# Optimization experiments

Hardware: AMD Instinct MI355X
Metric: run time of the kernel (lower is better)

Reference implementation:

```python
import jax, jax.numpy as jnp
import numpy as np

N_NODES = 50000
N_EDGES = 800000
IN_DIM = 128
HIDDEN = 128
OUT_DIM = 64


def setup_inputs() -> dict:
    key = jax.random.key(0)
    ks = jax.random.split(key, 10)
    x = jax.random.normal(ks[0], (N_NODES, IN_DIM), dtype=jnp.float32)
    edge_index = jax.random.randint(ks[1], (2, N_EDGES), 0, N_NODES, dtype=jnp.int64)
    def lin(k, fan_in, fan_out):
        bound = 1.0 / np.sqrt(fan_in)
        kw, kb = jax.random.split(k)
        W = jax.random.uniform(kw, (fan_in, fan_out), jnp.float32, -bound, bound)
        b = jax.random.uniform(kb, (fan_out,), jnp.float32, -bound, bound)
        return W, b
    W1, b1 = lin(ks[2], IN_DIM, HIDDEN)   # gcn layer 1
    W2, b2 = lin(ks[3], HIDDEN, HIDDEN)   # gcn layer 2
    W3, b3 = lin(ks[4], HIDDEN, HIDDEN)   # post_mp linear 1
    W4, b4 = lin(ks[5], HIDDEN, OUT_DIM)  # post_mp linear 2
    return {"x": x, "edge_index": edge_index,
            "W1": W1, "b1": b1, "W2": W2, "b2": b2,
            "W3": W3, "b3": b3, "W4": W4, "b4": b4}


def reference(x, edge_index, W1, b1, W2, b2, W3, b3, W4, b4):
    N = x.shape[0]
    # add self-loops (matches convert_to_adj)
    loops = jnp.arange(N, dtype=edge_index.dtype)
    row = jnp.concatenate([edge_index[0], loops])  # destination / adj row
    col = jnp.concatenate([edge_index[1], loops])  # source / adj col
    # row-normalization: vals = 1 / deg(row), deg from scatter-add of ones
    deg = jax.ops.segment_sum(jnp.ones(row.shape[0], x.dtype), row, num_segments=N)
    vals = 1.0 / deg[row]  # [E+N]

    def propagate(h):
        # SpMM: out[i] = sum_j A_norm[i,j] * h[j]  via gather-scale-scatter
        return jax.ops.segment_sum(vals[:, None] * h[col], row, num_segments=N)

    # layer 1: spmm -> linear -> relu (dropout is identity in eval mode)
    h = jax.nn.relu(propagate(x) @ W1 + b1)
    # layer 2
    h = jax.nn.relu(propagate(h) @ W2 + b2)
    # post_mp: Linear -> Dropout(eval=identity) -> Linear
    h = h @ W3 + b3
    return h @ W4 + b4
```

## Files before the change

kernel.cpp:

```cpp
#include <hip/hip_runtime.h>
#include <hip/hip_bf16.h>

#define NB 512

typedef __attribute__((ext_vector_type(8))) short short8_t;
typedef __attribute__((ext_vector_type(8))) unsigned short ushort8_t;
typedef __attribute__((ext_vector_type(4))) float f32x4;

__device__ inline unsigned short bf16_rne(float f) {
    union { float f; unsigned u; } x; x.f = f;
    unsigned r = x.u + 0x7fffu + ((x.u >> 16) & 1u);
    return (unsigned short)(r >> 16);
}
__device__ inline float bf16_to_f32(unsigned short h) {
    union { unsigned u; float f; } x; x.u = ((unsigned)h) << 16;
    return x.f;
}
__device__ __forceinline__ void acc_uint2(float& a0, float& a1, float& a2, float& a3, uint2 v) {
    a0 += bf16_to_f32((unsigned short)(v.x & 0xffff));
    a1 += bf16_to_f32((unsigned short)(v.x >> 16));
    a2 += bf16_to_f32((unsigned short)(v.y & 0xffff));
    a3 += bf16_to_f32((unsigned short)(v.y >> 16));
}


template <int NC, bool OUT_BF16>
__device__ __forceinline__ void gemm_core(const unsigned short* __restrict__ As,
                                          const unsigned short* __restrict__ Wt,
                                          const float* __restrict__ gemm_bias,
                                          void* __restrict__ Cout, int row0, int n) {
    constexpr int CT = NC / 32;
    const int t = threadIdx.x;
    const int w = t >> 6;
    const int l = t & 63;
    const int col = l & 15;
    const int kg = l >> 4;
    const int arow = (w & 3) * 16 + col;
    const int cbase = (w >> 2) * (NC / 2);
    const int abase = arow * 256;
    const int axor = (arow & 7) << 4;

    short8_t afrag[4];
#pragma unroll
    for (int ks = 0; ks < 4; ++ks) {
        int abyte = abase + ((ks * 64 + kg * 16) ^ axor);
        afrag[ks] = *(const short8_t*)((const char*)As + abyte);
    }

    f32x4 acc[CT];
#pragma unroll
    for (int ct = 0; ct < CT; ++ct) acc[ct] = (f32x4){0.f, 0.f, 0.f, 0.f};

#pragma unroll
    for (int ct = 0; ct < CT; ++ct) {
        const unsigned short* wp = Wt + (size_t)(cbase + ct * 16 + col) * 128 + kg * 8;
#pragma unroll
        for (int ks = 0; ks < 4; ++ks) {
            short8_t b = *(const short8_t*)(wp + ks * 32);
            acc[ct] = __builtin_amdgcn_mfma_f32_16x16x32_bf16(afrag[ks], b, acc[ct], 0, 0, 0);
        }
    }

    const int orow0 = row0 + (w & 3) * 16 + kg * 4;
    if (OUT_BF16) {
        unsigned short* C = (unsigned short*)Cout;
#pragma unroll
        for (int ct = 0; ct < CT; ++ct) {
#pragma unroll
            for (int j = 0; j < 4; ++j) {
                C[(size_t)(orow0 + j) * NC + cbase + ct * 16 + col] = bf16_rne(acc[ct][j]);
            }
        }
    } else {
        float* C = (float*)Cout;
#pragma unroll
        for (int ct = 0; ct < CT; ++ct) {
            float b = (gemm_bias != nullptr) ? gemm_bias[cbase + ct * 16 + col] : 0.f;
#pragma unroll
            for (int j = 0; j < 4; ++j) {
                int r = orow0 + j;
                if (r < n) C[(size_t)r * NC + cbase + ct * 16 + col] = acc[ct][j] + b;
            }
        }
    }
}


__global__ __launch_bounds__(512) void prep_p0_k(const int* __restrict__ e_row, int E, int R,
                                                 int* __restrict__ bucket_cnt, int pb,
                                                 const float* __restrict__ W1,
                                                 const float* __restrict__ W2,
                                                 const float* __restrict__ W3,
                                                 const float* __restrict__ b3,
                                                 const float* __restrict__ W4,
                                                 const float* __restrict__ b4,
                                                 unsigned short* __restrict__ w1t,
                                                 unsigned short* __restrict__ w2t,
                                                 unsigned short* __restrict__ wft,
                                                 float* __restrict__ bfv) {
    __shared__ int h[NB];
    if ((int)blockIdx.x < pb) {
        for (int i = threadIdx.x; i < NB; i += 512) h[i] = 0;
        __syncthreads();
        int base = blockIdx.x * 8192;
#pragma unroll
        for (int j = 0; j < 16; ++j) {
            int i = base + j * 512 + threadIdx.x;
            if (i < E) atomicAdd(&h[e_row[i] / R], 1);
        }
        __syncthreads();
        for (int i = threadIdx.x; i < NB; i += 512)
            if (h[i]) atomicAdd(&bucket_cnt[i], h[i]);
    } else {
        int idx = (blockIdx.x - pb) * 512 + threadIdx.x;
        if (idx < 16384) {
            int k = idx >> 7, c = idx & 127;
            w1t[c * 128 + k] = bf16_rne(W1[idx]);
        } else if (idx < 32768) {
            int j = idx - 16384;
            int k = j >> 7, c = j & 127;
            w2t[c * 128 + k] = bf16_rne(W2[j]);
        } else if (idx < 40960) {
            int j = idx - 32768;
            int k = j >> 6, o = j & 63;
            float acc = 0.f;
            for (int m = 0; m < 128; ++m) acc = fmaf(W3[k * 128 + m], W4[m * 64 + o], acc);
            wft[o * 128 + k] = bf16_rne(acc);
        } else if (idx < 41024) {
            int o = idx - 40960;
            float acc = b4[o];
            for (int m = 0; m < 128; ++m) acc = fmaf(b3[m], W4[m * 64 + o], acc);
            bfv[o] = acc;
        }
    }
}


__global__ __launch_bounds__(512) void gemm1_p0b_k(const float* __restrict__ x,
                                                   const unsigned short* __restrict__ w1t,
                                                   unsigned short* __restrict__ t1, int n, int gb,
                                                   const int* __restrict__ bucket_cnt,
                                                   int* __restrict__ bptr, int* __restrict__ bcur,
                                                   int E) {
    __shared__ char smem[16384];
    if ((int)blockIdx.x < gb) {
        unsigned short* As = (unsigned short*)smem;
        const int t = threadIdx.x;
        const int row0 = blockIdx.x * 64;
#pragma unroll
        for (int it = 0; it < 2; ++it) {
            int idx = it * 4096 + t * 8;
            int rl = idx >> 7;
            int cl = idx & 127;
            int gr = row0 + rl; if (gr > n - 1) gr = n - 1;
            const float4* src = (const float4*)(x + (size_t)gr * 128 + cl);
            float4 v0 = src[0];
            float4 v1 = src[1];
            float f[8] = {v0.x, v0.y, v0.z, v0.w, v1.x, v1.y, v1.z, v1.w};
            ushort8_t vh;
#pragma unroll
            for (int j = 0; j < 8; ++j) vh[j] = bf16_rne(f[j]);
            int byte = rl * 256 + ((cl * 2) ^ ((rl & 7) << 4));
            *(ushort8_t*)(smem + byte) = vh;
        }
        __syncthreads();
        gemm_core<128, true>(As, w1t, nullptr, t1, row0, n);
    } else {
        int* s = (int*)smem;
        int t = threadIdx.x;
        int v = bucket_cnt[t];
        s[t] = v;
        __syncthreads();
        for (int off = 1; off < NB; off <<= 1) {
            int u = (t >= off) ? s[t - off] : 0;
            __syncthreads();
            s[t] += u;
            __syncthreads();
        }
        int excl = s[t] - v;
        bptr[t] = excl;
        bcur[t] = excl;
        if (t == NB - 1) bptr[NB] = E;
    }
}


__global__ __launch_bounds__(256) void p1_scatter_k(const int* __restrict__ er,
                                                    const int* __restrict__ ec, int E, int R,
                                                    int* __restrict__ bcur,
                                                    unsigned* __restrict__ packed) {
    __shared__ int h[NB];
    __shared__ int base[NB];
    for (int i = threadIdx.x; i < NB; i += 256) h[i] = 0;
    __syncthreads();
    int cb = blockIdx.x * 4096;
    int rows[16], cols[16], bks[16];
#pragma unroll
    for (int j = 0; j < 16; ++j) {
        int i = cb + j * 256 + threadIdx.x;
        if (i < E) {
            int r = er[i];
            rows[j] = r;
            cols[j] = ec[i];
            int b = r / R;
            bks[j] = b;
            atomicAdd(&h[b], 1);
        } else {
            bks[j] = -1;
        }
    }
    __syncthreads();
    for (int i = threadIdx.x; i < NB; i += 256)
        base[i] = h[i] ? atomicAdd(&bcur[i], h[i]) : 0;
    __syncthreads();
    for (int i = threadIdx.x; i < NB; i += 256) h[i] = 0;
    __syncthreads();
#pragma unroll
    for (int j = 0; j < 16; ++j) {
        int b = bks[j];
        if (b >= 0) {
            int off = atomicAdd(&h[b], 1);
            packed[base[b] + off] = ((unsigned)(rows[j] - b * R) << 16) | (unsigned)cols[j];
        }
    }
}


__global__ __launch_bounds__(256) void p2_build_k(const unsigned* __restrict__ packed,
                                                  const int* __restrict__ bptr, int R, int N, int E,
                                                  int* __restrict__ row_ptr,
                                                  float* __restrict__ deginv,
                                                  int* __restrict__ csr_col) {
    __shared__ int hist[128];
    __shared__ int excl[129];
    __shared__ int cur[128];
    __shared__ int lcsr[2048];
    int b = blockIdx.x;
    int s = bptr[b], e = bptr[b + 1];
    int m = e - s;
    for (int i = threadIdx.x; i < 128; i += 256) hist[i] = 0;
    __syncthreads();
    for (int i = threadIdx.x; i < m; i += 256) atomicAdd(&hist[packed[s + i] >> 16], 1);
    __syncthreads();
    if (threadIdx.x == 0) {
        int acc = 0;
        for (int r = 0; r < R; ++r) { excl[r] = acc; acc += hist[r]; }
        excl[R] = acc;
    }
    __syncthreads();
    for (int r = threadIdx.x; r < R; r += 256) {
        int gr = b * R + r;
        if (gr < N) {
            row_ptr[gr] = s + excl[r];
            deginv[gr] = 1.0f / (float)(hist[r] + 1);
        }
        cur[r] = excl[r];
    }
    if (b == (int)gridDim.x - 1 && threadIdx.x == 0) row_ptr[N] = E;
    __syncthreads();
    if (m <= 2048) {
        for (int i = threadIdx.x; i < m; i += 256) {
            unsigned pk = packed[s + i];
            int pos = atomicAdd(&cur[pk >> 16], 1);
            lcsr[pos] = (int)(pk & 0xffffu);
        }
        __syncthreads();
        for (int i = threadIdx.x; i < m; i += 256) csr_col[s + i] = lcsr[i];
    } else {
        for (int i = threadIdx.x; i < m; i += 256) {
            unsigned pk = packed[s + i];
            int pos = atomicAdd(&cur[pk >> 16], 1);
            csr_col[s + pos] = (int)(pk & 0xffffu);
        }
    }
}


template <int NC, bool OUT_BF16>
__global__ __launch_bounds__(512) void fused_agg_gemm_k(const unsigned short* __restrict__ tin,
                                                        const int* __restrict__ row_ptr,
                                                        const int* __restrict__ csr_col,
                                                        const float* __restrict__ deginv,
                                                        const float* __restrict__ agg_bias,
                                                        const unsigned short* __restrict__ Wt,
                                                        const float* __restrict__ gemm_bias,
                                                        void* __restrict__ Cout, int n) {
    __shared__ unsigned short As[64 * 128];
    __shared__ int cols_s[2048];
    __shared__ int rp_s[65];
    __shared__ float di_s[64];
    const int t = threadIdx.x;
    const int row0 = blockIdx.x * 64;
    const int w = t >> 6;
    const int l = t & 63;
    const int half = l >> 5;
    const int sl = l & 31;
    const uint2* tw = (const uint2*)tin;
    const float4 bb = ((const float4*)agg_bias)[sl];

    if (t < 65) {
        int gr = row0 + t; if (gr > n) gr = n;
        rp_s[t] = row_ptr[gr];
    } else if (t < 129) {
        int gr = row0 + (t - 65); if (gr > n - 1) gr = n - 1;
        di_s[t - 65] = deginv[gr];
    }
    __syncthreads();
    const int seg0 = rp_s[0];
    {
        int seg_len = rp_s[64] - seg0;
        if (seg_len > 2048) seg_len = 2048;
        for (int i = t; i < seg_len; i += 512) cols_s[i] = csr_col[seg0 + i];
    }
    __syncthreads();

#pragma unroll
    for (int it = 0; it < 4; ++it) {
        int rl = it * 16 + w * 2 + half;
        int grow = row0 + rl; if (grow > n - 1) grow = n - 1;
        uint2 sv = tw[(size_t)grow * 32 + sl];
        float a0 = bf16_to_f32((unsigned short)(sv.x & 0xffff));
        float a1 = bf16_to_f32((unsigned short)(sv.x >> 16));
        float a2 = bf16_to_f32((unsigned short)(sv.y & 0xffff));
        float a3 = bf16_to_f32((unsigned short)(sv.y >> 16));
        const int s = rp_s[rl], e = rp_s[rl + 1];
        const int d = e - s;
        if (e - seg0 <= 2048) {
            const int loc = s - seg0;
            int p = 0;
            for (; p + 8 <= d; p += 8) {
                int c0 = cols_s[loc + p + 0];
                int c1 = cols_s[loc + p + 1];
                int c2 = cols_s[loc + p + 2];
                int c3 = cols_s[loc + p + 3];
                int c4 = cols_s[loc + p + 4];
                int c5 = cols_s[loc + p + 5];
                int c6 = cols_s[loc + p + 6];
                int c7 = cols_s[loc + p + 7];
                uint2 v0 = tw[(size_t)c0 * 32 + sl];
                uint2 v1 = tw[(size_t)c1 * 32 + sl];
                uint2 v2 = tw[(size_t)c2 * 32 + sl];
                uint2 v3 = tw[(size_t)c3 * 32 + sl];
                uint2 v4 = tw[(size_t)c4 * 32 + sl];
                uint2 v5 = tw[(size_t)c5 * 32 + sl];
                uint2 v6 = tw[(size_t)c6 * 32 + sl];
                uint2 v7 = tw[(size_t)c7 * 32 + sl];
                acc_uint2(a0, a1, a2, a3, v0);
                acc_uint2(a0, a1, a2, a3, v1);
                acc_uint2(a0, a1, a2, a3, v2);
                acc_uint2(a0, a1, a2, a3, v3);
                acc_uint2(a0, a1, a2, a3, v4);
                acc_uint2(a0, a1, a2, a3, v5);
                acc_uint2(a0, a1, a2, a3, v6);
                acc_uint2(a0, a1, a2, a3, v7);
            }
            for (; p < d; ++p) {
                int c = cols_s[loc + p];
                uint2 v = tw[(size_t)c * 32 + sl];
                acc_uint2(a0, a1, a2, a3, v);
            }
        } else {
            for (int p = s; p < e; ++p) {
                int c = csr_col[p];
                uint2 v = tw[(size_t)c * 32 + sl];
                acc_uint2(a0, a1, a2, a3, v);
            }
        }
        float di = di_s[rl];
        float r0 = fmaxf(fmaf(a0, di, bb.x), 0.f);
        float r1 = fmaxf(fmaf(a1, di, bb.y), 0.f);
        float r2 = fmaxf(fmaf(a2, di, bb.z), 0.f);
        float r3 = fmaxf(fmaf(a3, di, bb.w), 0.f);
        uint2 pk;
        pk.x = (unsigned)bf16_rne(r0) | ((unsigned)bf16_rne(r1) << 16);
        pk.y = (unsigned)bf16_rne(r2) | ((unsigned)bf16_rne(r3) << 16);
        int byte = rl * 256 + ((sl * 8) ^ ((rl & 7) << 4));
        *(uint2*)((char*)As + byte) = pk;
    }
    __syncthreads();

    gemm_core<NC, OUT_BF16>(As, Wt, gemm_bias, Cout, row0, n);
}


extern "C" void kernel_launch(void* const* d_in, const int* in_sizes, int n_in,
                              void* d_out, int out_size, void* d_ws, size_t ws_size,
                              hipStream_t stream) {
    const float* x  = (const float*)d_in[0];
    const int* edges = (const int*)d_in[1];
    const float* W1 = (const float*)d_in[2];
    const float* b1 = (const float*)d_in[3];
    const float* W2 = (const float*)d_in[4];
    const float* b2 = (const float*)d_in[5];
    const float* W3 = (const float*)d_in[6];
    const float* b3 = (const float*)d_in[7];
    const float* W4 = (const float*)d_in[8];
    const float* b4 = (const float*)d_in[9];

    const int N = in_sizes[0] / 128;
    const int E = in_sizes[1] / 2;
    const int NPAD = (N + 63) & ~63;
    const int R = (N + NB - 1) / NB;
    const int* e_row = edges;
    const int* e_col = edges + E;

    char* p = (char*)d_ws;
    auto alloc = [&](size_t bytes) {
        void* r = (void*)p;
        p += (bytes + 255) & ~(size_t)255;
        return r;
    };
    unsigned short* t_bf = (unsigned short*)alloc((size_t)NPAD * 128 * 2);
    unsigned short* t2_bf = (unsigned short*)alloc((size_t)NPAD * 128 * 2);
    float* deginv  = (float*)alloc((size_t)N * 4);
    int*   row_ptr = (int*)alloc((size_t)(N + 1) * 4);
    int*   csr_col = (int*)alloc((size_t)E * 4);
    unsigned* packed = (unsigned*)alloc((size_t)E * 4);
    int*   bucket_cnt = (int*)alloc(NB * 4);
    int*   bucket_ptr = (int*)alloc((NB + 1) * 4);
    int*   bucket_cur = (int*)alloc(NB * 4);
    unsigned short* w1t = (unsigned short*)alloc(128 * 128 * 2);
    unsigned short* w2t = (unsigned short*)alloc(128 * 128 * 2);
    unsigned short* wft = (unsigned short*)alloc(64 * 128 * 2);
    float* bfv     = (float*)alloc(64 * 4);

    float* out = (float*)d_out;

    hipMemsetAsync(bucket_cnt, 0, NB * 4, stream);

    const int PB = (E + 8191) / 8192;
    const int WB = (41024 + 511) / 512;
    const int gblocks = NPAD / 64;

    prep_p0_k<<<PB + WB, 512, 0, stream>>>(e_row, E, R, bucket_cnt, PB,
                                           W1, W2, W3, b3, W4, b4, w1t, w2t, wft, bfv);
    gemm1_p0b_k<<<gblocks + 1, 512, 0, stream>>>(x, w1t, t_bf, N, gblocks,
                                                 bucket_cnt, bucket_ptr, bucket_cur, E);
    p1_scatter_k<<<(E + 4095) / 4096, 256, 0, stream>>>(e_row, e_col, E, R, bucket_cur, packed);
    p2_build_k<<<NB, 256, 0, stream>>>(packed, bucket_ptr, R, N, E, row_ptr, deginv, csr_col);

    fused_agg_gemm_k<128, true><<<gblocks, 512, 0, stream>>>(
        t_bf, row_ptr, csr_col, deginv, b1, w2t, nullptr, t2_bf, N);
    fused_agg_gemm_k<64, false><<<gblocks, 512, 0, stream>>>(
        t2_bf, row_ptr, csr_col, deginv, b2, wft, bfv, out, N);
}
```

Measured before the change: 221.3 us.

## Partition CSR by source-column chunk to improve gather locality

Edges are bucketed by source-column chunk (4 chunks of 12800 nodes) as well as by destination row block. This produces four per-chunk row pointer arrays, so aggregation walks neighbours chunk by chunk and its gathers concentrate on a smaller slice of the feature table at a time, aiming for better L2 reuse. Degree inverse is now computed inline from the summed chunk degrees instead of being stored, and the gather loop uses two accumulator sets. It adds more buckets, a larger scan, extra row-pointer loads, and a hardcoded chunk size that assumes N at most 51200.

Result: slower. 270.7 us (+22.3%).

```diff
diff --git a/kernel.cpp b/kernel.cpp
--- a/kernel.cpp
+++ b/kernel.cpp
@@ -2,6 +2,9 @@
 #include <hip/hip_bf16.h>
 
 #define NB 512
+#define NCHUNK 4
+#define NBK (NB * NCHUNK)
+#define CHUNK_ROWS 12800
 
 typedef __attribute__((ext_vector_type(8))) short short8_t;
 typedef __attribute__((ext_vector_type(8))) unsigned short ushort8_t;
@@ -86,7 +89,8 @@
 }
 
 
-__global__ __launch_bounds__(512) void prep_p0_k(const int* __restrict__ e_row, int E, int R,
+__global__ __launch_bounds__(512) void prep_p0_k(const int* __restrict__ e_row,
+                                                 const int* __restrict__ e_col, int E, int R,
                                                  int* __restrict__ bucket_cnt, int pb,
                                                  const float* __restrict__ W1,
                                                  const float* __restrict__ W2,
@@ -98,18 +102,21 @@
                                                  unsigned short* __restrict__ w2t,
                                                  unsigned short* __restrict__ wft,
                                                  float* __restrict__ bfv) {
-    __shared__ int h[NB];
+    __shared__ int h[NBK];
     if ((int)blockIdx.x < pb) {
-        for (int i = threadIdx.x; i < NB; i += 512) h[i] = 0;
+        for (int i = threadIdx.x; i < NBK; i += 512) h[i] = 0;
         __syncthreads();
         int base = blockIdx.x * 8192;
 #pragma unroll
         for (int j = 0; j < 16; ++j) {
             int i = base + j * 512 + threadIdx.x;
-            if (i < E) atomicAdd(&h[e_row[i] / R], 1);
+            if (i < E) {
+                int bk = (e_col[i] / CHUNK_ROWS) * NB + e_row[i] / R;
+                atomicAdd(&h[bk], 1);
+            }
         }
         __syncthreads();
-        for (int i = threadIdx.x; i < NB; i += 512)
+        for (int i = threadIdx.x; i < NBK; i += 512)
             if (h[i]) atomicAdd(&bucket_cnt[i], h[i]);
     } else {
         int idx = (blockIdx.x - pb) * 512 + threadIdx.x;
@@ -168,41 +175,49 @@
     } else {
         int* s = (int*)smem;
         int t = threadIdx.x;
-        int v = bucket_cnt[t];
-        s[t] = v;
+        int t4 = t * 4;
+        int v0 = bucket_cnt[t4 + 0];
+        int v1 = bucket_cnt[t4 + 1];
+        int v2 = bucket_cnt[t4 + 2];
+        int v3 = bucket_cnt[t4 + 3];
+        int tsum = v0 + v1 + v2 + v3;
+        s[t] = tsum;
         __syncthreads();
-        for (int off = 1; off < NB; off <<= 1) {
+        for (int off = 1; off < 512; off <<= 1) {
             int u = (t >= off) ? s[t - off] : 0;
             __syncthreads();
             s[t] += u;
             __syncthreads();
         }
-        int excl = s[t] - v;
-        bptr[t] = excl;
-        bcur[t] = excl;
-        if (t == NB - 1) bptr[NB] = E;
-    }
-}
-
-
-__global__ __launch_bounds__(256) void p1_scatter_k(const int* __restrict__ er,
+        int excl = s[t] - tsum;
+        bptr[t4 + 0] = excl;            bcur[t4 + 0] = excl;
+        bptr[t4 + 1] = excl + v0;       bcur[t4 + 1] = excl + v0;
+        bptr[t4 + 2] = excl + v0 + v1;  bcur[t4 + 2] = excl + v0 + v1;
+        bptr[t4 + 3] = excl + v0 + v1 + v2; bcur[t4 + 3] = excl + v0 + v1 + v2;
+        if (t == 511) bptr[NBK] = E;
+    }
+}
+
+
+__global__ __launch_bounds__(512) void p1_scatter_k(const int* __restrict__ er,
                                                     const int* __restrict__ ec, int E, int R,
                                                     int* __restrict__ bcur,
                                                     unsigned* __restrict__ packed) {
-    __shared__ int h[NB];
-    __shared__ int base[NB];
-    for (int i = threadIdx.x; i < NB; i += 256) h[i] = 0;
-    __syncthreads();
-    int cb = blockIdx.x * 4096;
+    __shared__ int h[NBK];
+    __shared__ int base[NBK];
+    for (int i = threadIdx.x; i < NBK; i += 512) h[i] = 0;
+    __syncthreads();
+    int cb = blockIdx.x * 8192;
     int rows[16], cols[16], bks[16];
 #pragma unroll
     for (int j = 0; j < 16; ++j) {
-        int i = cb + j * 256 + threadIdx.x;
+        int i = cb + j * 512 + threadIdx.x;
         if (i < E) {
             int r = er[i];
+            int c = ec[i];
             rows[j] = r;
-            cols[j] = ec[i];
-            int b = r / R;
+            cols[j] = c;
+            int b = (c / CHUNK_ROWS) * NB + r / R;
             bks[j] = b;
             atomicAdd(&h[b], 1);
         } else {
@@ -210,17 +225,18 @@
         }
     }
     __syncthreads();
-    for (int i = threadIdx.x; i < NB; i += 256)
+    for (int i = threadIdx.x; i < NBK; i += 512)
         base[i] = h[i] ? atomicAdd(&bcur[i], h[i]) : 0;
     __syncthreads();
-    for (int i = threadIdx.x; i < NB; i += 256) h[i] = 0;
+    for (int i = threadIdx.x; i < NBK; i += 512) h[i] = 0;
     __syncthreads();
 #pragma unroll
     for (int j = 0; j < 16; ++j) {
         int b = bks[j];
         if (b >= 0) {
             int off = atomicAdd(&h[b], 1);
-            packed[base[b] + off] = ((unsigned)(rows[j] - b * R) << 16) | (unsigned)cols[j];
+            int localrow = rows[j] - (b & (NB - 1)) * R;
+            packed[base[b] + off] = ((unsigned)localrow << 16) | (unsigned)cols[j];
         }
     }
 }
@@ -228,14 +244,15 @@
 
 __global__ __launch_bounds__(256) void p2_build_k(const unsigned* __restrict__ packed,
                                                   const int* __restrict__ bptr, int R, int N, int E,
-                                                  int* __restrict__ row_ptr,
-                                                  float* __restrict__ deginv,
+                                                  int* __restrict__ rp2,
                                                   int* __restrict__ csr_col) {
     __shared__ int hist[128];
     __shared__ int excl[129];
     __shared__ int cur[128];
     __shared__ int lcsr[2048];
     int b = blockIdx.x;
+    int c = b / NB;
+    int rb = b & (NB - 1);
     int s = bptr[b], e = bptr[b + 1];
     int m = e - s;
     for (int i = threadIdx.x; i < 128; i += 256) hist[i] = 0;
@@ -249,14 +266,11 @@
     }
     __syncthreads();
     for (int r = threadIdx.x; r < R; r += 256) {
-        int gr = b * R + r;
-        if (gr < N) {
-            row_ptr[gr] = s + excl[r];
-            deginv[gr] = 1.0f / (float)(hist[r] + 1);
-        }
+        int gr = rb * R + r;
+        if (gr < N) rp2[(size_t)c * N + gr] = s + excl[r];
         cur[r] = excl[r];
     }
-    if (b == (int)gridDim.x - 1 && threadIdx.x == 0) row_ptr[N] = E;
+    if (b == NBK - 1 && threadIdx.x == 0) rp2[(size_t)NCHUNK * N] = E;
     __syncthreads();
     if (m <= 2048) {
         for (int i = threadIdx.x; i < m; i += 256) {
@@ -278,17 +292,15 @@
 
 template <int NC, bool OUT_BF16>
 __global__ __launch_bounds__(512) void fused_agg_gemm_k(const unsigned short* __restrict__ tin,
-                                                        const int* __restrict__ row_ptr,
+                                                        const int* __restrict__ rp2,
                                                         const int* __restrict__ csr_col,
-                                                        const float* __restrict__ deginv,
                                                         const float* __restrict__ agg_bias,
                                                         const unsigned short* __restrict__ Wt,
                                                         const float* __restrict__ gemm_bias,
                                                         void* __restrict__ Cout, int n) {
     __shared__ unsigned short As[64 * 128];
     __shared__ int cols_s[2048];
-    __shared__ int rp_s[65];
-    __shared__ float di_s[64];
+    __shared__ int rp_s[NCHUNK][65];
     const int t = threadIdx.x;
     const int row0 = blockIdx.x * 64;
     const int w = t >> 6;
@@ -298,19 +310,26 @@
     const uint2* tw = (const uint2*)tin;
     const float4 bb = ((const float4*)agg_bias)[sl];
 
-    if (t < 65) {
-        int gr = row0 + t; if (gr > n) gr = n;
-        rp_s[t] = row_ptr[gr];
-    } else if (t < 129) {
-        int gr = row0 + (t - 65); if (gr > n - 1) gr = n - 1;
-        di_s[t - 65] = deginv[gr];
-    }
-    __syncthreads();
-    const int seg0 = rp_s[0];
-    {
-        int seg_len = rp_s[64] - seg0;
-        if (seg_len > 2048) seg_len = 2048;
-        for (int i = t; i < seg_len; i += 512) cols_s[i] = csr_col[seg0 + i];
+    if (t < NCHUNK * 65) {
+        int c = t / 65, i = t - c * 65;
+        int mi = row0 + i; if (mi > n) mi = n;
+        rp_s[c][i] = rp2[(size_t)c * n + mi];
+    }
+    __syncthreads();
+
+    int off_c[NCHUNK + 1];
+    off_c[0] = 0;
+#pragma unroll
+    for (int c = 0; c < NCHUNK; ++c) off_c[c + 1] = off_c[c] + (rp_s[c][64] - rp_s[c][0]);
+    const bool staged = off_c[NCHUNK] <= 2048;
+    if (staged) {
+#pragma unroll
+        for (int c = 0; c < NCHUNK; ++c) {
+            int s0 = rp_s[c][0];
+            int len = rp_s[c][64] - s0;
+            int o = off_c[c];
+            for (int i = t; i < len; i += 512) cols_s[o + i] = csr_col[s0 + i];
+        }
     }
     __syncthreads();
 
@@ -323,50 +342,45 @@
         float a1 = bf16_to_f32((unsigned short)(sv.x >> 16));
         float a2 = bf16_to_f32((unsigned short)(sv.y & 0xffff));
         float a3 = bf16_to_f32((unsigned short)(sv.y >> 16));
-        const int s = rp_s[rl], e = rp_s[rl + 1];
-        const int d = e - s;
-        if (e - seg0 <= 2048) {
-            const int loc = s - seg0;
-            int p = 0;
-            for (; p + 8 <= d; p += 8) {
-                int c0 = cols_s[loc + p + 0];
-                int c1 = cols_s[loc + p + 1];
-                int c2 = cols_s[loc + p + 2];
-                int c3 = cols_s[loc + p + 3];
-                int c4 = cols_s[loc + p + 4];
-                int c5 = cols_s[loc + p + 5];
-                int c6 = cols_s[loc + p + 6];
-                int c7 = cols_s[loc + p + 7];
-                uint2 v0 = tw[(size_t)c0 * 32 + sl];
-                uint2 v1 = tw[(size_t)c1 * 32 + sl];
-                uint2 v2 = tw[(size_t)c2 * 32 + sl];
-                uint2 v3 = tw[(size_t)c3 * 32 + sl];
-                uint2 v4 = tw[(size_t)c4 * 32 + sl];
-                uint2 v5 = tw[(size_t)c5 * 32 + sl];
-                uint2 v6 = tw[(size_t)c6 * 32 + sl];
-                uint2 v7 = tw[(size_t)c7 * 32 + sl];
-                acc_uint2(a0, a1, a2, a3, v0);
-                acc_uint2(a0, a1, a2, a3, v1);
-                acc_uint2(a0, a1, a2, a3, v2);
-                acc_uint2(a0, a1, a2, a3, v3);
-                acc_uint2(a0, a1, a2, a3, v4);
-                acc_uint2(a0, a1, a2, a3, v5);
-                acc_uint2(a0, a1, a2, a3, v6);
-                acc_uint2(a0, a1, a2, a3, v7);
+        float b0 = 0.f, b1 = 0.f, b2 = 0.f, b3v = 0.f;
+        int dtot = 0;
+#pragma unroll
+        for (int c = 0; c < NCHUNK; ++c) {
+            const int s = rp_s[c][rl], e = rp_s[c][rl + 1];
+            const int d = e - s;
+            dtot += d;
+            if (staged) {
+                const int base = off_c[c] + (s - rp_s[c][0]);
+                int p = 0;
+                for (; p + 4 <= d; p += 4) {
+                    int c0 = cols_s[base + p + 0];
+                    int c1 = cols_s[base + p + 1];
+                    int c2 = cols_s[base + p + 2];
+                    int c3 = cols_s[base + p + 3];
+                    uint2 v0 = tw[(size_t)c0 * 32 + sl];
+                    uint2 v1 = tw[(size_t)c1 * 32 + sl];
+                    uint2 v2 = tw[(size_t)c2 * 32 + sl];
+                    uint2 v3 = tw[(size_t)c3 * 32 + sl];
+                    acc_uint2(a0, a1, a2, a3, v0);
+                    acc_uint2(b0, b1, b2, b3v, v1);
+                    acc_uint2(a0, a1, a2, a3, v2);
+                    acc_uint2(b0, b1, b2, b3v, v3);
+                }
+                for (; p < d; ++p) {
+                    int cc = cols_s[base + p];
+                    uint2 v = tw[(size_t)cc * 32 + sl];
+                    acc_uint2(a0, a1, a2, a3, v);
+                }
+            } else {
+                for (int p = s; p < e; ++p) {
+                    int cc = csr_col[p];
+                    uint2 v = tw[(size_t)cc * 32 + sl];
+                    acc_uint2(a0, a1, a2, a3, v);
+                }
             }
-            for (; p < d; ++p) {
-                int c = cols_s[loc + p];
-                uint2 v = tw[(size_t)c * 32 + sl];
-                acc_uint2(a0, a1, a2, a3, v);
-            }
-        } else {
-            for (int p = s; p < e; ++p) {
-                int c = csr_col[p];
-                uint2 v = tw[(size_t)c * 32 + sl];
-                acc_uint2(a0, a1, a2, a3, v);
-            }
-        }
-        float di = di_s[rl];
+        }
+        a0 += b0; a1 += b1; a2 += b2; a3 += b3v;
+        float di = 1.0f / (float)(dtot + 1);
         float r0 = fmaxf(fmaf(a0, di, bb.x), 0.f);
         float r1 = fmaxf(fmaf(a1, di, bb.y), 0.f);
         float r2 = fmaxf(fmaf(a2, di, bb.z), 0.f);
@@ -412,13 +426,12 @@
     };
     unsigned short* t_bf = (unsigned short*)alloc((size_t)NPAD * 128 * 2);
     unsigned short* t2_bf = (unsigned short*)alloc((size_t)NPAD * 128 * 2);
-    float* deginv  = (float*)alloc((size_t)N * 4);
-    int*   row_ptr = (int*)alloc((size_t)(N + 1) * 4);
+    int*   rp2     = (int*)alloc(((size_t)NCHUNK * N + 1) * 4);
     int*   csr_col = (int*)alloc((size_t)E * 4);
     unsigned* packed = (unsigned*)alloc((size_t)E * 4);
-    int*   bucket_cnt = (int*)alloc(NB * 4);
-    int*   bucket_ptr = (int*)alloc((NB + 1) * 4);
-    int*   bucket_cur = (int*)alloc(NB * 4);
+    int*   bucket_cnt = (int*)alloc(NBK * 4);
+    int*   bucket_ptr = (int*)alloc((NBK + 1) * 4);
+    int*   bucket_cur = (int*)alloc(NBK * 4);
     unsigned short* w1t = (unsigned short*)alloc(128 * 128 * 2);
     unsigned short* w2t = (unsigned short*)alloc(128 * 128 * 2);
     unsigned short* wft = (unsigned short*)alloc(64 * 128 * 2);
@@ -426,21 +439,21 @@
 
     float* out = (float*)d_out;
 
-    hipMemsetAsync(bucket_cnt, 0, NB * 4, stream);
+    hipMemsetAsync(bucket_cnt, 0, NBK * 4, stream);
 
     const int PB = (E + 8191) / 8192;
     const int WB = (41024 + 511) / 512;
     const int gblocks = NPAD / 64;
 
-    prep_p0_k<<<PB + WB, 512, 0, stream>>>(e_row, E, R, bucket_cnt, PB,
+    prep_p0_k<<<PB + WB, 512, 0, stream>>>(e_row, e_col, E, R, bucket_cnt, PB,
                                            W1, W2, W3, b3, W4, b4, w1t, w2t, wft, bfv);
     gemm1_p0b_k<<<gblocks + 1, 512, 0, stream>>>(x, w1t, t_bf, N, gblocks,
                                                  bucket_cnt, bucket_ptr, bucket_cur, E);
-    p1_scatter_k<<<(E + 4095) / 4096, 256, 0, stream>>>(e_row, e_col, E, R, bucket_cur, packed);
-    p2_build_k<<<NB, 256, 0, stream>>>(packed, bucket_ptr, R, N, E, row_ptr, deginv, csr_col);
+    p1_scatter_k<<<(E + 8191) / 8192, 512, 0, stream>>>(e_row, e_col, E, R, bucket_cur, packed);
+    p2_build_k<<<NBK, 256, 0, stream>>>(packed, bucket_ptr, R, N, E, rp2, csr_col);
 
     fused_agg_gemm_k<128, true><<<gblocks, 512, 0, stream>>>(
-        t_bf, row_ptr, csr_col, deginv, b1, w2t, nullptr, t2_bf, N);
+        t_bf, rp2, csr_col, b1, w2t, nullptr, t2_bf, N);
     fused_agg_gemm_k<64, false><<<gblocks, 512, 0, stream>>>(
-        t2_bf, row_ptr, csr_col, deginv, b2, wft, bfv, out, N);
-}
+        t2_bf, rp2, csr_col, b2, wft, bfv, out, N);
+}
```

## Split fused aggregate-GEMM into slab-layout aggregation and separate GEMM kernels

Applied to the files above, without the earlier changes.

Stores the bf16 node features in four 32-column slabs (feature-group major) so each aggregation block gathers only 64-byte rows of one slab, which may improve cache locality of the random neighbour gathers. The fused aggregate+GEMM kernel is replaced by a separate aggregation kernel (four blocks per 64-row tile, one per slab) and a GEMM kernel that loads the slab tile into LDS with global_load_lds. This adds two extra launches and a round trip of the hidden activations through global memory, and it gathers the column indices four times.

Measured after the change: 231.3 us. 1.05x slower.

```diff
diff --git a/kernel.cpp b/kernel.cpp
--- a/kernel.cpp
+++ b/kernel.cpp
@@ -24,11 +24,11 @@
 }
 
 
-template <int NC, bool OUT_BF16>
+template <int NC, bool OUT_SLAB, bool SLAB_A>
 __device__ __forceinline__ void gemm_core(const unsigned short* __restrict__ As,
                                           const unsigned short* __restrict__ Wt,
                                           const float* __restrict__ gemm_bias,
-                                          void* __restrict__ Cout, int row0, int n) {
+                                          void* __restrict__ Cout, int row0, int n, int npad) {
     constexpr int CT = NC / 32;
     const int t = threadIdx.x;
     const int w = t >> 6;
@@ -37,13 +37,13 @@
     const int kg = l >> 4;
     const int arow = (w & 3) * 16 + col;
     const int cbase = (w >> 2) * (NC / 2);
-    const int abase = arow * 256;
-    const int axor = (arow & 7) << 4;
 
     short8_t afrag[4];
 #pragma unroll
     for (int ks = 0; ks < 4; ++ks) {
-        int abyte = abase + ((ks * 64 + kg * 16) ^ axor);
+        int abyte;
+        if (SLAB_A) abyte = ks * 4096 + arow * 64 + kg * 16;
+        else        abyte = arow * 256 + ((ks * 64 + kg * 16) ^ ((arow & 7) << 4));
         afrag[ks] = *(const short8_t*)((const char*)As + abyte);
     }
 
@@ -62,13 +62,15 @@
     }
 
     const int orow0 = row0 + (w & 3) * 16 + kg * 4;
-    if (OUT_BF16) {
+    if (OUT_SLAB) {
         unsigned short* C = (unsigned short*)Cout;
 #pragma unroll
         for (int ct = 0; ct < CT; ++ct) {
+            int f = cbase + ct * 16 + col;
+            unsigned short* slab = C + (size_t)(f >> 5) * npad * 32 + (f & 31);
 #pragma unroll
             for (int j = 0; j < 4; ++j) {
-                C[(size_t)(orow0 + j) * NC + cbase + ct * 16 + col] = bf16_rne(acc[ct][j]);
+                slab[(size_t)(orow0 + j) * 32] = bf16_rne(acc[ct][j]);
             }
         }
     } else {
@@ -138,8 +140,8 @@
 
 __global__ __launch_bounds__(512) void gemm1_p0b_k(const float* __restrict__ x,
                                                    const unsigned short* __restrict__ w1t,
-                                                   unsigned short* __restrict__ t1, int n, int gb,
-                                                   const int* __restrict__ bucket_cnt,
+                                                   unsigned short* __restrict__ t1, int n, int npad,
+                                                   int gb, const int* __restrict__ bucket_cnt,
                                                    int* __restrict__ bptr, int* __restrict__ bcur,
                                                    int E) {
     __shared__ char smem[16384];
@@ -164,7 +166,7 @@
             *(ushort8_t*)(smem + byte) = vh;
         }
         __syncthreads();
-        gemm_core<128, true>(As, w1t, nullptr, t1, row0, n);
+        gemm_core<128, true, false>(As, w1t, nullptr, t1, row0, n, npad);
     } else {
         int* s = (int*)smem;
         int t = threadIdx.x;
@@ -276,27 +278,19 @@
 }
 
 
-template <int NC, bool OUT_BF16>
-__global__ __launch_bounds__(512) void fused_agg_gemm_k(const unsigned short* __restrict__ tin,
-                                                        const int* __restrict__ row_ptr,
-                                                        const int* __restrict__ csr_col,
-                                                        const float* __restrict__ deginv,
-                                                        const float* __restrict__ agg_bias,
-                                                        const unsigned short* __restrict__ Wt,
-                                                        const float* __restrict__ gemm_bias,
-                                                        void* __restrict__ Cout, int n) {
-    __shared__ unsigned short As[64 * 128];
+__global__ __launch_bounds__(256) void agg_slab_k(const unsigned short* __restrict__ tin,
+                                                  const int* __restrict__ row_ptr,
+                                                  const int* __restrict__ csr_col,
+                                                  const float* __restrict__ deginv,
+                                                  const float* __restrict__ agg_bias,
+                                                  unsigned short* __restrict__ hout,
+                                                  int n, int npad) {
     __shared__ int cols_s[2048];
     __shared__ int rp_s[65];
     __shared__ float di_s[64];
+    const int g = blockIdx.x & 3;
+    const int row0 = (blockIdx.x >> 2) * 64;
     const int t = threadIdx.x;
-    const int row0 = blockIdx.x * 64;
-    const int w = t >> 6;
-    const int l = t & 63;
-    const int half = l >> 5;
-    const int sl = l & 31;
-    const uint2* tw = (const uint2*)tin;
-    const float4 bb = ((const float4*)agg_bias)[sl];
 
     if (t < 65) {
         int gr = row0 + t; if (gr > n) gr = n;
@@ -307,66 +301,65 @@
     }
     __syncthreads();
     const int seg0 = rp_s[0];
-    {
-        int seg_len = rp_s[64] - seg0;
-        if (seg_len > 2048) seg_len = 2048;
-        for (int i = t; i < seg_len; i += 512) cols_s[i] = csr_col[seg0 + i];
-    }
-    __syncthreads();
-
-#pragma unroll
-    for (int it = 0; it < 4; ++it) {
-        int rl = it * 16 + w * 2 + half;
-        int grow = row0 + rl; if (grow > n - 1) grow = n - 1;
-        uint2 sv = tw[(size_t)grow * 32 + sl];
+    const int seg_len = rp_s[64] - seg0;
+    const bool staged = seg_len <= 2048;
+    if (staged) {
+        for (int i = t; i < seg_len; i += 256) cols_s[i] = csr_col[seg0 + i];
+    }
+    __syncthreads();
+
+    const uint2* tg = (const uint2*)(tin + (size_t)g * npad * 32);
+    uint2* hg = (uint2*)(hout + (size_t)g * npad * 32);
+    const int w = t >> 6;
+    const int l = t & 63;
+    const int o = l >> 3;
+    const int fl = l & 7;
+    const float4 bb = ((const float4*)agg_bias)[g * 8 + fl];
+
+#pragma unroll
+    for (int pass = 0; pass < 2; ++pass) {
+        const int rl = pass * 32 + w * 8 + o;
+        const int grow = row0 + rl;
+        const int crow = (grow > n - 1) ? (n - 1) : grow;
+        uint2 sv = tg[(size_t)crow * 8 + fl];
         float a0 = bf16_to_f32((unsigned short)(sv.x & 0xffff));
         float a1 = bf16_to_f32((unsigned short)(sv.x >> 16));
         float a2 = bf16_to_f32((unsigned short)(sv.y & 0xffff));
         float a3 = bf16_to_f32((unsigned short)(sv.y >> 16));
+        float b0 = 0.f, b1 = 0.f, b2 = 0.f, b3v = 0.f;
         const int s = rp_s[rl], e = rp_s[rl + 1];
         const int d = e - s;
-        if (e - seg0 <= 2048) {
+        if (staged) {
             const int loc = s - seg0;
             int p = 0;
-            for (; p + 8 <= d; p += 8) {
+            for (; p + 4 <= d; p += 4) {
                 int c0 = cols_s[loc + p + 0];
                 int c1 = cols_s[loc + p + 1];
                 int c2 = cols_s[loc + p + 2];
                 int c3 = cols_s[loc + p + 3];
-                int c4 = cols_s[loc + p + 4];
-                int c5 = cols_s[loc + p + 5];
-                int c6 = cols_s[loc + p + 6];
-                int c7 = cols_s[loc + p + 7];
-                uint2 v0 = tw[(size_t)c0 * 32 + sl];
-                uint2 v1 = tw[(size_t)c1 * 32 + sl];
-                uint2 v2 = tw[(size_t)c2 * 32 + sl];
-                uint2 v3 = tw[(size_t)c3 * 32 + sl];
-                uint2 v4 = tw[(size_t)c4 * 32 + sl];
-                uint2 v5 = tw[(size_t)c5 * 32 + sl];
-                uint2 v6 = tw[(size_t)c6 * 32 + sl];
-                uint2 v7 = tw[(size_t)c7 * 32 + sl];
+                uint2 v0 = tg[(size_t)c0 * 8 + fl];
+                uint2 v1 = tg[(size_t)c1 * 8 + fl];
+                uint2 v2 = tg[(size_t)c2 * 8 + fl];
+                uint2 v3 = tg[(size_t)c3 * 8 + fl];
                 acc_uint2(a0, a1, a2, a3, v0);
-                acc_uint2(a0, a1, a2, a3, v1);
+                acc_uint2(b0, b1, b2, b3v, v1);
                 acc_uint2(a0, a1, a2, a3, v2);
-                acc_uint2(a0, a1, a2, a3, v3);
-                acc_uint2(a0, a1, a2, a3, v4);
-                acc_uint2(a0, a1, a2, a3, v5);
-                acc_uint2(a0, a1, a2, a3, v6);
-                acc_uint2(a0, a1, a2, a3, v7);
+                acc_uint2(b0, b1, b2, b3v, v3);
             }
             for (; p < d; ++p) {
                 int c = cols_s[loc + p];
-                uint2 v = tw[(size_t)c * 32 + sl];
+                uint2 v = tg[(size_t)c * 8 + fl];
                 acc_uint2(a0, a1, a2, a3, v);
             }
         } else {
             for (int p = s; p < e; ++p) {
                 int c = csr_col[p];
-                uint2 v = tw[(size_t)c * 32 + sl];
+                uint2 v = tg[(size_t)c * 8 + fl];
                 acc_uint2(a0, a1, a2, a3, v);
             }
         }
-        float di = di_s[rl];
+        a0 += b0; a1 += b1; a2 += b2; a3 += b3v;
+        const float di = di_s[rl];
         float r0 = fmaxf(fmaf(a0, di, bb.x), 0.f);
         float r1 = fmaxf(fmaf(a1, di, bb.y), 0.f);
         float r2 = fmaxf(fmaf(a2, di, bb.z), 0.f);
@@ -374,12 +367,32 @@
         uint2 pk;
         pk.x = (unsigned)bf16_rne(r0) | ((unsigned)bf16_rne(r1) << 16);
         pk.y = (unsigned)bf16_rne(r2) | ((unsigned)bf16_rne(r3) << 16);
-        int byte = rl * 256 + ((sl * 8) ^ ((rl & 7) << 4));
-        *(uint2*)((char*)As + byte) = pk;
-    }
-    __syncthreads();
-
-    gemm_core<NC, OUT_BF16>(As, Wt, gemm_bias, Cout, row0, n);
+        hg[(size_t)grow * 8 + fl] = pk;
+    }
+}
+
+
+template <int NC, bool OUT_SLAB>
+__global__ __launch_bounds__(512) void gemm_slab_k(const unsigned short* __restrict__ A,
+                                                   const unsigned short* __restrict__ Wt,
+                                                   const float* __restrict__ gemm_bias,
+                                                   void* __restrict__ Cout, int n, int npad) {
+    __shared__ unsigned short As[64 * 128];
+    const int t = threadIdx.x;
+    const int row0 = blockIdx.x * 64;
+    const char* base = (const char*)A;
+#pragma unroll
+    for (int it = 0; it < 2; ++it) {
+        int dst = it * 8192 + t * 16;
+        int s = dst >> 12;
+        int o = dst & 4095;
+        const char* src = base + (size_t)s * npad * 64 + (size_t)row0 * 64 + o;
+        __builtin_amdgcn_global_load_lds(
+            (const __attribute__((address_space(1))) void*)src,
+            (__attribute__((address_space(3))) void*)((char*)As + dst), 16, 0, 0);
+    }
+    __syncthreads();
+    gemm_core<NC, OUT_SLAB, true>(As, Wt, gemm_bias, Cout, row0, n, npad);
 }
 
 
@@ -410,8 +423,8 @@
         p += (bytes + 255) & ~(size_t)255;
         return r;
     };
-    unsigned short* t_bf = (unsigned short*)alloc((size_t)NPAD * 128 * 2);
-    unsigned short* t2_bf = (unsigned short*)alloc((size_t)NPAD * 128 * 2);
+    unsigned short* t_sl = (unsigned short*)alloc((size_t)NPAD * 128 * 2);
+    unsigned short* h_sl = (unsigned short*)alloc((size_t)NPAD * 128 * 2);
     float* deginv  = (float*)alloc((size_t)N * 4);
     int*   row_ptr = (int*)alloc((size_t)(N + 1) * 4);
     int*   csr_col = (int*)alloc((size_t)E * 4);
@@ -434,13 +447,13 @@
 
     prep_p0_k<<<PB + WB, 512, 0, stream>>>(e_row, E, R, bucket_cnt, PB,
                                            W1, W2, W3, b3, W4, b4, w1t, w2t, wft, bfv);
-    gemm1_p0b_k<<<gblocks + 1, 512, 0, stream>>>(x, w1t, t_bf, N, gblocks,
+    gemm1_p0b_k<<<gblocks + 1, 512, 0, stream>>>(x, w1t, t_sl, N, NPAD, gblocks,
                                                  bucket_cnt, bucket_ptr, bucket_cur, E);
     p1_scatter_k<<<(E + 4095) / 4096, 256, 0, stream>>>(e_row, e_col, E, R, bucket_cur, packed);
     p2_build_k<<<NB, 256, 0, stream>>>(packed, bucket_ptr, R, N, E, row_ptr, deginv, csr_col);
 
-    fused_agg_gemm_k<128, true><<<gblocks, 512, 0, stream>>>(
-        t_bf, row_ptr, csr_col, deginv, b1, w2t, nullptr, t2_bf, N);
-    fused_agg_gemm_k<64, false><<<gblocks, 512, 0, stream>>>(
-        t2_bf, row_ptr, csr_col, deginv, b2, wft, bfv, out, N);
-}
+    agg_slab_k<<<4 * gblocks, 256, 0, stream>>>(t_sl, row_ptr, csr_col, deginv, b1, h_sl, N, NPAD);
+    gemm_slab_k<128, true><<<gblocks, 512, 0, stream>>>(h_sl, w2t, nullptr, t_sl, N, NPAD);
+    agg_slab_k<<<4 * gblocks, 256, 0, stream>>>(t_sl, row_ptr, csr_col, deginv, b2, h_sl, N, NPAD);
+    gemm_slab_k<64, false><<<gblocks, 512, 0, stream>>>(h_sl, wft, bfv, out, N, NPAD);
+}
```
